# Optimization experiments

Hardware: AMD Instinct MI355X
Metric: run time of the kernel (lower is better)

## Reference

```python
import jax, jax.numpy as jnp
import numpy as np

N = 100000        # nodes
E = 1600000       # edges
G = 128           # graphs in batch
D_FEAT = 240      # continuous node features (input_features - 1)
EMB = 16          # node-type embedding dim
H = 256           # hidden size (both layers)
PH = 128          # pool / classifier hidden
GF = 32           # global feature dim
LN_EPS = 1e-5


def setup_inputs() -> dict:
    key = jax.random.key(0)
    ks = jax.random.split(key, 24)

    node_types = jax.random.randint(ks[0], (N,), 0, 400).astype(jnp.float32)
    feats = jax.random.normal(ks[1], (N, D_FEAT), dtype=jnp.float32)
    x = jnp.concatenate([node_types[:, None], feats], axis=1)  # [N, 241]

    edge_index = jax.random.randint(ks[2], (2, E), 0, N, dtype=jnp.int32)
    batch = jnp.sort(jax.random.randint(ks[3], (N,), 0, G, dtype=jnp.int32))
    global_features = jax.random.normal(ks[4], (G, GF), dtype=jnp.float32)

    s = 0.05
    p = {}
    p['emb_table'] = jax.random.normal(ks[5], (400, EMB), dtype=jnp.float32) * s
    # layer 0 GIN MLP (in=256 -> 256 -> 256) + LayerNorm
    p['l0_w1'] = jax.random.normal(ks[6], (H, H), dtype=jnp.float32) * s
    p['l0_b1'] = jnp.zeros((H,), jnp.float32)
    p['l0_w2'] = jax.random.normal(ks[7], (H, H), dtype=jnp.float32) * s
    p['l0_b2'] = jnp.zeros((H,), jnp.float32)
    p['ln0_g'] = jnp.ones((H,), jnp.float32)
    p['ln0_b'] = jnp.zeros((H,), jnp.float32)
    # layer 1
    p['l1_w1'] = jax.random.normal(ks[8], (H, H), dtype=jnp.float32) * s
    p['l1_b1'] = jnp.zeros((H,), jnp.float32)
    p['l1_w2'] = jax.random.normal(ks[9], (H, H), dtype=jnp.float32) * s
    p['l1_b2'] = jnp.zeros((H,), jnp.float32)
    p['ln1_g'] = jnp.ones((H,), jnp.float32)
    p['ln1_b'] = jnp.zeros((H,), jnp.float32)
    # attentional aggregation gate: 256 -> 128 -> 1
    p['gate_w1'] = jax.random.normal(ks[10], (H, PH), dtype=jnp.float32) * s
    p['gate_b1'] = jnp.zeros((PH,), jnp.float32)
    p['gate_w2'] = jax.random.normal(ks[11], (PH, 1), dtype=jnp.float32) * s
    p['gate_b2'] = jnp.zeros((1,), jnp.float32)
    # classifier: 256+32 -> 128 -> 2
    p['cls_w1'] = jax.random.normal(ks[12], (H + GF, PH), dtype=jnp.float32) * s
    p['cls_b1'] = jnp.zeros((PH,), jnp.float32)
    p['cls_w2'] = jax.random.normal(ks[13], (PH, 2), dtype=jnp.float32) * s
    p['cls_b2'] = jnp.zeros((2,), jnp.float32)

    return dict(x=x, edge_index=edge_index, batch=batch,
                global_features=global_features, **p)


def _layernorm(z, g, b):
    mu = jnp.mean(z, axis=-1, keepdims=True)
    var = jnp.mean(jnp.square(z - mu), axis=-1, keepdims=True)
    return (z - mu) * jax.lax.rsqrt(var + LN_EPS) * g + b


def _gin_block(h, src, dst, w1, b1, w2, b2, ln_g, ln_b):
    # GINConv, eps=0: mlp((1+eps)*x_i + sum_{j->i} x_j)
    agg = jax.ops.segment_sum(h[src], dst, num_segments=h.shape[0])
    z = h + agg
    z = jax.nn.relu(z @ w1 + b1) @ w2 + b2
    z = jax.nn.relu(_layernorm(z, ln_g, ln_b))
    return h + z  # dropout is identity in eval; residual


def reference(x, edge_index, batch, global_features, emb_table,
              l0_w1, l0_b1, l0_w2, l0_b2, ln0_g, ln0_b,
              l1_w1, l1_b1, l1_w2, l1_b2, ln1_g, ln1_b,
              gate_w1, gate_b1, gate_w2, gate_b2,
              cls_w1, cls_b1, cls_w2, cls_b2):
    node_types = x[:, 0].astype(jnp.int32)
    h = jnp.concatenate([x[:, 1:], emb_table[node_types]], axis=1)  # [N, 256]

    src, dst = edge_index[0], edge_index[1]
    h = _gin_block(h, src, dst, l0_w1, l0_b1, l0_w2, l0_b2, ln0_g, ln0_b)
    h = _gin_block(h, src, dst, l1_w1, l1_b1, l1_w2, l1_b2, ln1_g, ln1_b)

    # AttentionalAggregation: segment softmax over gate scores, weighted sum
    gate = jax.nn.relu(h @ gate_w1 + gate_b1) @ gate_w2 + gate_b2  # [N, 1]
    gate = gate[:, 0]
    m = jax.ops.segment_max(gate, batch, num_segments=G)
    a = jnp.exp(gate - m[batch])
    s = jax.ops.segment_sum(a, batch, num_segments=G)
    w = a / s[batch]
    pooled = jax.ops.segment_sum(w[:, None] * h, batch, num_segments=G)  # [G, 256]

    z = jnp.concatenate([pooled, global_features], axis=1)  # [G, 288]
    out = jax.nn.relu(z @ cls_w1 + cls_b1) @ cls_w2 + cls_b2  # [G, 2]
    return out
```

## Files before the change

### kernel.cpp

```cpp
#include <hip/hip_runtime.h>
#include <math.h>

#define N_NODES 100000
#define N_EDGES 1600000
#define NG      128
#define HD      256
#define PHD     128
#define GFD     32
#define XW      241
#define LN_EPS  1e-5f
#define SLOT    64

typedef __attribute__((ext_vector_type(8))) short bf8_t;
typedef __attribute__((ext_vector_type(4))) float f4_t;

static __device__ __forceinline__ float relu_f(float x){ return fmaxf(x, 0.0f); }

static __device__ __forceinline__ unsigned short f2bf_rn(float v) {
    unsigned int u = __float_as_uint(v);
    unsigned int r = (u + 0x7fffu + ((u >> 16) & 1u)) >> 16;
    return (unsigned short)r;
}
static __device__ __forceinline__ float bf2f(unsigned short h) {
    return __uint_as_float((unsigned int)h << 16);
}

__global__ void build_h_kernel(const float* __restrict__ x, const float* __restrict__ emb,
                               float* __restrict__ h, unsigned short* __restrict__ h16)
{
    int node = blockIdx.x;
    int tid  = threadIdx.x;
    const float* xr = x + (size_t)node * XW;
    float v;
    if (tid < 240) {
        v = xr[1 + tid];
    } else {
        int t = (int)xr[0];
        v = emb[t * 16 + (tid - 240)];
    }
    h[(size_t)node * HD + tid] = v;
    h16[(size_t)node * HD + tid] = f2bf_rn(v);
}

__global__ void fill_slots_kernel(const int* __restrict__ src, const int* __restrict__ dst,
                                  int* __restrict__ cnt, int* __restrict__ col, int e)
{
    int i = blockIdx.x * blockDim.x + threadIdx.x;
    if (i < e) {
        int d = dst[i];
        int p = atomicAdd(&cnt[d], 1);
        if (p < SLOT) col[(size_t)d * SLOT + p] = src[i];
    }
}

static __device__ __forceinline__ void pack_one(const float* __restrict__ w, short* __restrict__ hi,
                                                int N, int fbase)
{
    int lane = threadIdx.x & 63;
    int f = fbase * 4 + (threadIdx.x >> 6);
    const int KB = 8;
    int nb = f / KB, kb = f % KB;
    int n = nb * 16 + (lane & 15);
    int k0 = kb * 32 + (lane >> 4) * 8;
    size_t o = (size_t)f * 512 + lane * 8;
    #pragma unroll
    for (int j = 0; j < 8; j++) {
        float v = w[(size_t)(k0 + j) * N + n];
        hi[o + j] = (short)f2bf_rn(v);
    }
}

__global__ __launch_bounds__(256) void pack_all_kernel(
    const float* __restrict__ w0, const float* __restrict__ w1,
    const float* __restrict__ w2, const float* __restrict__ w3,
    const float* __restrict__ w4,
    short* o0h, short* o1h, short* o2h, short* o3h, short* o4h)
{
    int b = blockIdx.x;
    if      (b < 32)  pack_one(w0, o0h, HD,  b);
    else if (b < 64)  pack_one(w1, o1h, HD,  b - 32);
    else if (b < 96)  pack_one(w2, o2h, HD,  b - 64);
    else if (b < 128) pack_one(w3, o3h, HD,  b - 96);
    else              pack_one(w4, o4h, PHD, b - 128);
}

static __device__ __forceinline__ void mm32(
    f4_t (&acc)[2][4], const char* buf,
    const short* __restrict__ Bh,
    int wc, int cb, int kg, int lane)
{
    bf8_t bcur[4], bnxt[4];
    #pragma unroll
    for (int ni = 0; ni < 4; ni++)
        bcur[ni] = *(const bf8_t*)&Bh[((size_t)((wc*4+ni)*8))*512 + lane*8];
    for (int kb = 0; kb < 8; kb++) {
        if (kb < 7) {
            #pragma unroll
            for (int ni = 0; ni < 4; ni++)
                bnxt[ni] = *(const bf8_t*)&Bh[((size_t)((wc*4+ni)*8 + kb+1))*512 + lane*8];
        }
        bf8_t ahi[2], alo[2];
        #pragma unroll
        for (int mi = 0; mi < 2; mi++) {
            int row = mi*16 + cb;
            int byte = (row*512 + kb*64 + kg*16) ^ ((row & 7) << 4);
            ahi[mi] = *(const bf8_t*)(buf + byte);
            alo[mi] = *(const bf8_t*)(buf + 16384 + byte);
        }
        #pragma unroll
        for (int mi = 0; mi < 2; mi++)
            #pragma unroll
            for (int ni = 0; ni < 4; ni++)
                acc[mi][ni] = __builtin_amdgcn_mfma_f32_16x16x32_bf16(ahi[mi], bcur[ni], acc[mi][ni], 0, 0, 0);
        #pragma unroll
        for (int mi = 0; mi < 2; mi++)
            #pragma unroll
            for (int ni = 0; ni < 4; ni++)
                acc[mi][ni] = __builtin_amdgcn_mfma_f32_16x16x32_bf16(alo[mi], bcur[ni], acc[mi][ni], 0, 0, 0);
        #pragma unroll
        for (int ni = 0; ni < 4; ni++) bcur[ni] = bnxt[ni];
    }
}

__global__ __launch_bounds__(256, 4) void gin_layer_kernel(
    float* __restrict__ h, const unsigned short* __restrict__ h16i,
    unsigned short* __restrict__ h16o,
    const int* __restrict__ cnt, const int* __restrict__ col,
    const short* __restrict__ w1h, const float* __restrict__ b1,
    const short* __restrict__ w2h, const float* __restrict__ b2,
    const float* __restrict__ lng, const float* __restrict__ lnb)
{
    __shared__ char buf[32768];
    const int tid  = threadIdx.x;
    const int lane = tid & 63;
    const int wv   = tid >> 6;
    const int cb   = lane & 15;
    const int kg   = lane >> 4;
    const int l4   = lane * 4;
    const long row0 = (long)blockIdx.x * 32;

    for (int rr = 0; rr < 8; rr++) {
        int row = wv * 8 + rr;
        long grow = row0 + row;
        float4 a0 = *(const float4*)&h[grow * HD + l4];
        float4 a1 = make_float4(0,0,0,0), a2 = make_float4(0,0,0,0), a3 = make_float4(0,0,0,0);
        int deg = cnt[grow]; if (deg > SLOT) deg = SLOT;
        const int* cb4 = col + (size_t)grow * SLOT;
        int e = 0;
        for (; e + 4 <= deg; e += 4) {
            int s0 = cb4[e], s1 = cb4[e+1], s2 = cb4[e+2], s3 = cb4[e+3];
            ushort4 u0 = *(const ushort4*)&h16i[(size_t)s0 * HD + l4];
            ushort4 u1 = *(const ushort4*)&h16i[(size_t)s1 * HD + l4];
            ushort4 u2 = *(const ushort4*)&h16i[(size_t)s2 * HD + l4];
            ushort4 u3 = *(const ushort4*)&h16i[(size_t)s3 * HD + l4];
            a0.x += bf2f(u0.x); a0.y += bf2f(u0.y); a0.z += bf2f(u0.z); a0.w += bf2f(u0.w);
            a1.x += bf2f(u1.x); a1.y += bf2f(u1.y); a1.z += bf2f(u1.z); a1.w += bf2f(u1.w);
            a2.x += bf2f(u2.x); a2.y += bf2f(u2.y); a2.z += bf2f(u2.z); a2.w += bf2f(u2.w);
            a3.x += bf2f(u3.x); a3.y += bf2f(u3.y); a3.z += bf2f(u3.z); a3.w += bf2f(u3.w);
        }
        for (; e < deg; e++) {
            int s = cb4[e];
            ushort4 u = *(const ushort4*)&h16i[(size_t)s * HD + l4];
            a0.x += bf2f(u.x); a0.y += bf2f(u.y); a0.z += bf2f(u.z); a0.w += bf2f(u.w);
        }
        a0.x += a1.x + a2.x + a3.x;
        a0.y += a1.y + a2.y + a3.y;
        a0.z += a1.z + a2.z + a3.z;
        a0.w += a1.w + a2.w + a3.w;
        ushort4 hi4, lo4;
        unsigned short hb;
        hb = f2bf_rn(a0.x); hi4.x = hb; lo4.x = f2bf_rn(a0.x - bf2f(hb));
        hb = f2bf_rn(a0.y); hi4.y = hb; lo4.y = f2bf_rn(a0.y - bf2f(hb));
        hb = f2bf_rn(a0.z); hi4.z = hb; lo4.z = f2bf_rn(a0.z - bf2f(hb));
        hb = f2bf_rn(a0.w); hi4.w = hb; lo4.w = f2bf_rn(a0.w - bf2f(hb));
        int byte = (row * 512 + lane * 8) ^ ((row & 7) << 4);
        *(ushort4*)(buf + byte)         = hi4;
        *(ushort4*)(buf + 16384 + byte) = lo4;
    }
    __syncthreads();

    f4_t acc[2][4];
    const f4_t zero4 = {0.f, 0.f, 0.f, 0.f};
    #pragma unroll
    for (int mi = 0; mi < 2; mi++)
        #pragma unroll
        for (int ni = 0; ni < 4; ni++) acc[mi][ni] = zero4;

    mm32(acc, buf, w1h, wv, cb, kg, lane);
    __syncthreads();

    {
        float bias1[4];
        #pragma unroll
        for (int ni = 0; ni < 4; ni++) bias1[ni] = b1[wv * 64 + ni * 16 + cb];
        #pragma unroll
        for (int mi = 0; mi < 2; mi++) {
            #pragma unroll
            for (int ni = 0; ni < 4; ni++) {
                int colx2 = (wv * 64 + ni * 16 + cb) * 2;
                #pragma unroll
                for (int j = 0; j < 4; j++) {
                    float t = relu_f(acc[mi][ni][j] + bias1[ni]);
                    int row = mi * 16 + kg * 4 + j;
                    unsigned short hb = f2bf_rn(t);
                    unsigned short lb = f2bf_rn(t - bf2f(hb));
                    int byte = (row * 512 + colx2) ^ ((row & 7) << 4);
                    *(short*)(buf + byte)         = (short)hb;
                    *(short*)(buf + 16384 + byte) = (short)lb;
                }
            }
        }
    }
    __syncthreads();

    #pragma unroll
    for (int mi = 0; mi < 2; mi++)
        #pragma unroll
        for (int ni = 0; ni < 4; ni++) acc[mi][ni] = zero4;

    mm32(acc, buf, w2h, wv, cb, kg, lane);
    __syncthreads();

    {
        float bias2[4];
        #pragma unroll
        for (int ni = 0; ni < 4; ni++) bias2[ni] = b2[wv * 64 + ni * 16 + cb];
        #pragma unroll
        for (int mi = 0; mi < 2; mi++) {
            #pragma unroll
            for (int ni = 0; ni < 4; ni++) {
                int col2 = wv * 64 + ni * 16 + cb;
                #pragma unroll
                for (int j = 0; j < 4; j++) {
                    int row = mi * 16 + kg * 4 + j;
                    int byte = (row * 1024 + col2 * 4) ^ (((row >> 2) & 3) << 6);
                    *(float*)(buf + byte) = acc[mi][ni][j] + bias2[ni];
                }
            }
        }
    }
    __syncthreads();

    {
        const float4 gv = *(const float4*)&lng[l4];
        const float4 bv = *(const float4*)&lnb[l4];
        for (int rr = 0; rr < 8; rr++) {
            int row = wv * 8 + rr;
            long grow = row0 + row;
            int byte = (row * 1024 + lane * 16) ^ (((row >> 2) & 3) << 6);
            float4 v = *(const float4*)(buf + byte);
            float s = v.x + v.y + v.z + v.w;
            float q = v.x * v.x + v.y * v.y + v.z * v.z + v.w * v.w;
            #pragma unroll
            for (int off = 32; off > 0; off >>= 1) {
                s += __shfl_xor(s, off, 64);
                q += __shfl_xor(q, off, 64);
            }
            float mu = s * (1.0f / 256.0f);
            float var = q * (1.0f / 256.0f) - mu * mu;
            float rstd = rsqrtf(var + LN_EPS);
            size_t gi = (size_t)grow * HD + l4;
            float4 hv = *(float4*)&h[gi];
            hv.x += relu_f((v.x - mu) * rstd * gv.x + bv.x);
            hv.y += relu_f((v.y - mu) * rstd * gv.y + bv.y);
            hv.z += relu_f((v.z - mu) * rstd * gv.z + bv.z);
            hv.w += relu_f((v.w - mu) * rstd * gv.w + bv.w);
            *(float4*)&h[gi] = hv;
            ushort4 m16;
            m16.x = f2bf_rn(hv.x); m16.y = f2bf_rn(hv.y);
            m16.z = f2bf_rn(hv.z); m16.w = f2bf_rn(hv.w);
            *(ushort4*)&h16o[gi] = m16;
        }
    }
}

__global__ __launch_bounds__(256, 2) void gate_mfma_kernel(
    const float* __restrict__ h,
    const short* __restrict__ g1h, const float* __restrict__ gb1,
    const float* __restrict__ gw2, const float* __restrict__ gb2,
    float* __restrict__ gate)
{
    __shared__ char buf[65536];
    const int tid  = threadIdx.x;
    const int lane = tid & 63;
    const int wv   = tid >> 6;
    const int cb   = lane & 15;
    const int kg   = lane >> 4;
    const long row0 = (long)blockIdx.x * 64;

    for (int rr = 0; rr < 16; rr++) {
        int row = wv * 16 + rr;
        long grow = row0 + row;
        float4 v = make_float4(0.f, 0.f, 0.f, 0.f);
        if (grow < N_NODES) v = *(const float4*)&h[grow * HD + lane * 4];
        ushort4 hi4, lo4;
        unsigned short hb;
        hb = f2bf_rn(v.x); hi4.x = hb; lo4.x = f2bf_rn(v.x - bf2f(hb));
        hb = f2bf_rn(v.y); hi4.y = hb; lo4.y = f2bf_rn(v.y - bf2f(hb));
        hb = f2bf_rn(v.z); hi4.z = hb; lo4.z = f2bf_rn(v.z - bf2f(hb));
        hb = f2bf_rn(v.w); hi4.w = hb; lo4.w = f2bf_rn(v.w - bf2f(hb));
        int byte = (row * 512 + lane * 8) ^ ((row & 7) << 4);
        *(ushort4*)(buf + byte)         = hi4;
        *(ushort4*)(buf + 32768 + byte) = lo4;
    }
    __syncthreads();

    f4_t acc[4][2];
    const f4_t zero4 = {0.f, 0.f, 0.f, 0.f};
    #pragma unroll
    for (int mi = 0; mi < 4; mi++) { acc[mi][0] = zero4; acc[mi][1] = zero4; }

    #pragma unroll
    for (int pass = 0; pass < 2; pass++) {
        const char* Abase = (pass == 1) ? (buf + 32768) : buf;
        for (int kb = 0; kb < 8; kb++) {
            bf8_t a[4], b[2];
            #pragma unroll
            for (int mi = 0; mi < 4; mi++) {
                int row = mi * 16 + cb;
                int byte = (row * 512 + kb * 64 + kg * 16) ^ ((row & 7) << 4);
                a[mi] = *(const bf8_t*)(Abase + byte);
            }
            #pragma unroll
            for (int ni = 0; ni < 2; ni++) {
                int nb = wv * 2 + ni;
                b[ni] = *(const bf8_t*)&g1h[(size_t)(nb * 8 + kb) * 512 + lane * 8];
            }
            #pragma unroll
            for (int mi = 0; mi < 4; mi++)
                #pragma unroll
                for (int ni = 0; ni < 2; ni++)
                    acc[mi][ni] = __builtin_amdgcn_mfma_f32_16x16x32_bf16(a[mi], b[ni], acc[mi][ni], 0, 0, 0);
        }
    }
    __syncthreads();

    {
        float* G1 = (float*)buf;
        float bias1[2];
        bias1[0] = gb1[wv * 32 + cb];
        bias1[1] = gb1[wv * 32 + 16 + cb];
        #pragma unroll
        for (int mi = 0; mi < 4; mi++) {
            #pragma unroll
            for (int ni = 0; ni < 2; ni++) {
                int colv = wv * 32 + ni * 16 + cb;
                #pragma unroll
                for (int j = 0; j < 4; j++) {
                    int row = mi * 16 + kg * 4 + j;
                    G1[row * PHD + colv] = relu_f(acc[mi][ni][j] + bias1[ni]);
                }
            }
        }
    }
    __syncthreads();

    {
        const float* G1 = (const float*)buf;
        float2 wv2 = *(const float2*)&gw2[lane * 2];
        float b2v = gb2[0];
        for (int rr = 0; rr < 16; rr++) {
            int row = wv * 16 + rr;
            long grow = row0 + row;
            if (grow >= N_NODES) break;
            float2 t2 = *(const float2*)&G1[row * PHD + lane * 2];
            float p = t2.x * wv2.x + t2.y * wv2.y;
            #pragma unroll
            for (int off = 32; off > 0; off >>= 1) p += __shfl_xor(p, off, 64);
            if (lane == 0) gate[grow] = p + b2v;
        }
    }
}

__global__ void goff_kernel(const int* __restrict__ batch, int* __restrict__ goff, int n)
{
    int t = threadIdx.x;
    if (t > NG) return;
    int lo = 0, hi = n;
    while (lo < hi) {
        int mid = (lo + hi) >> 1;
        if (batch[mid] < t) lo = mid + 1; else hi = mid;
    }
    goff[t] = lo;
}

__global__ __launch_bounds__(256) void pool_kernel(
    const float* __restrict__ h, const float* __restrict__ gate,
    const int* __restrict__ goff, float* __restrict__ pooled)
{
    __shared__ float red[256];
    __shared__ float m_sh, s_sh;
    int g = blockIdx.x >> 2, q = blockIdx.x & 3;
    int tid = threadIdx.x;
    int beg = goff[g], end = goff[g + 1];
    if (beg >= end) return;

    float lm = -3.4e38f;
    for (int i = beg + tid; i < end; i += 256) lm = fmaxf(lm, gate[i]);
    red[tid] = lm; __syncthreads();
    for (int off = 128; off > 0; off >>= 1) {
        if (tid < off) red[tid] = fmaxf(red[tid], red[tid + off]);
        __syncthreads();
    }
    if (tid == 0) m_sh = red[0];
    __syncthreads();
    float m = m_sh;

    float ls = 0.0f;
    for (int i = beg + tid; i < end; i += 256) ls += expf(gate[i] - m);
    __syncthreads();
    red[tid] = ls; __syncthreads();
    for (int off = 128; off > 0; off >>= 1) {
        if (tid < off) red[tid] += red[tid + off];
        __syncthreads();
    }
    if (tid == 0) s_sh = red[0];
    __syncthreads();
    float inv_s = 1.0f / s_sh;

    float acc = 0.0f;
    for (int i = beg + q; i < end; i += 4) {
        float a = expf(gate[i] - m);
        acc += a * h[(size_t)i * HD + tid];
    }
    atomicAdd(&pooled[(size_t)g * HD + tid], acc * inv_s);
}

__global__ __launch_bounds__(128) void cls_kernel(
    const float* __restrict__ pooled, const float* __restrict__ gf,
    const float* __restrict__ w1, const float* __restrict__ b1,
    const float* __restrict__ w2, const float* __restrict__ b2,
    float* __restrict__ out)
{
    __shared__ float r0[128], r1[128];
    int g = blockIdx.x, c = threadIdx.x;
    float acc = b1[c];
    const float* pr = pooled + (size_t)g * HD;
    for (int k = 0; k < HD; k++) acc += pr[k] * w1[k * PHD + c];
    const float* gr = gf + g * GFD;
    for (int k = 0; k < GFD; k++) acc += gr[k] * w1[(HD + k) * PHD + c];
    float t = relu_f(acc);
    r0[c] = t * w2[c * 2 + 0];
    r1[c] = t * w2[c * 2 + 1];
    __syncthreads();
    for (int off = 64; off > 0; off >>= 1) {
        if (c < off) { r0[c] += r0[c + off]; r1[c] += r1[c + off]; }
        __syncthreads();
    }
    if (c == 0) {
        out[g * 2 + 0] = r0[0] + b2[0];
        out[g * 2 + 1] = r1[0] + b2[1];
    }
}

extern "C" void kernel_launch(void* const* d_in, const int* in_sizes, int n_in,
                              void* d_out, int out_size, void* d_ws, size_t ws_size,
                              hipStream_t stream)
{
    const float* x    = (const float*)d_in[0];
    const int*   ei   = (const int*)d_in[1];
    const int*   bat  = (const int*)d_in[2];
    const float* gf   = (const float*)d_in[3];
    const float* emb  = (const float*)d_in[4];
    const float* l0w1 = (const float*)d_in[5];
    const float* l0b1 = (const float*)d_in[6];
    const float* l0w2 = (const float*)d_in[7];
    const float* l0b2 = (const float*)d_in[8];
    const float* ln0g = (const float*)d_in[9];
    const float* ln0b = (const float*)d_in[10];
    const float* l1w1 = (const float*)d_in[11];
    const float* l1b1 = (const float*)d_in[12];
    const float* l1w2 = (const float*)d_in[13];
    const float* l1b2 = (const float*)d_in[14];
    const float* ln1g = (const float*)d_in[15];
    const float* ln1b = (const float*)d_in[16];
    const float* gw1  = (const float*)d_in[17];
    const float* gb1  = (const float*)d_in[18];
    const float* gw2  = (const float*)d_in[19];
    const float* gb2  = (const float*)d_in[20];
    const float* cw1  = (const float*)d_in[21];
    const float* cb1  = (const float*)d_in[22];
    const float* cw2  = (const float*)d_in[23];
    const float* cb2  = (const float*)d_in[24];

    char* ws = (char*)d_ws;
    size_t off = 0;
    auto alloc = [&](size_t bytes) {
        void* p = ws + off;
        off += (bytes + 255) & ~(size_t)255;
        return p;
    };
    float* h      = (float*)alloc((size_t)N_NODES * HD * 4);
    unsigned short* h16a = (unsigned short*)alloc((size_t)N_NODES * HD * 2);
    unsigned short* h16b = (unsigned short*)alloc((size_t)N_NODES * HD * 2);
    float* gate   = (float*)alloc((size_t)N_NODES * 4);
    int*   cnt    = (int*)alloc((size_t)N_NODES * 4);
    int*   col    = (int*)alloc((size_t)N_NODES * SLOT * 4);
    int*   goff   = (int*)alloc((NG + 1) * 4);
    float* pooled = (float*)alloc((size_t)NG * HD * 4);
    short* p_l0w1h = (short*)alloc((size_t)HD * HD * 2);
    short* p_l0w2h = (short*)alloc((size_t)HD * HD * 2);
    short* p_l1w1h = (short*)alloc((size_t)HD * HD * 2);
    short* p_l1w2h = (short*)alloc((size_t)HD * HD * 2);
    short* p_gw1h  = (short*)alloc((size_t)HD * PHD * 2);

    const int* src = ei;
    const int* dst = ei + N_EDGES;

    build_h_kernel<<<N_NODES, 256, 0, stream>>>(x, emb, h, h16a);

    hipMemsetAsync(cnt, 0, (size_t)N_NODES * 4, stream);
    fill_slots_kernel<<<(N_EDGES + 255) / 256, 256, 0, stream>>>(src, dst, cnt, col, N_EDGES);

    pack_all_kernel<<<144, 256, 0, stream>>>(l0w1, l0w2, l1w1, l1w2, gw1,
                                             p_l0w1h, p_l0w2h, p_l1w1h, p_l1w2h, p_gw1h);

    const int layer_grid = N_NODES / 32;

    gin_layer_kernel<<<layer_grid, 256, 0, stream>>>(h, h16a, h16b, cnt, col,
                                                     p_l0w1h, l0b1, p_l0w2h, l0b2, ln0g, ln0b);
    gin_layer_kernel<<<layer_grid, 256, 0, stream>>>(h, h16b, h16a, cnt, col,
                                                     p_l1w1h, l1b1, p_l1w2h, l1b2, ln1g, ln1b);

    gate_mfma_kernel<<<(N_NODES + 63) / 64, 256, 0, stream>>>(h, p_gw1h, gb1, gw2, gb2, gate);
    goff_kernel<<<1, 256, 0, stream>>>(bat, goff, N_NODES);
    hipMemsetAsync(pooled, 0, (size_t)NG * HD * 4, stream);
    pool_kernel<<<NG * 4, 256, 0, stream>>>(h, gate, goff, pooled);
    cls_kernel<<<NG, 128, 0, stream>>>(pooled, gf, cw1, cb1, cw2, cb2, (float*)d_out);
}
```

Before: 769.7 us.

## Use single-bf16 pass for second GIN matmul and raise occupancy bound

The intermediate activation after the first MLP layer is now stored as a single bf16 value instead of a hi/lo bf16 split, and the second matmul uses a new one-pass MFMA routine, halving MFMA work and LDS traffic for that GEMM. Launch bounds move from 4 to 5 blocks per CU to allow more occupancy, and the CSR slot fill uses nontemporal stores. The trade is reduced accuracy in the second matmul and possible register pressure from the tighter launch bound.

```diff
diff --git a/kernel.cpp b/kernel.cpp
--- a/kernel.cpp
+++ b/kernel.cpp
@@ -49,7 +49,7 @@
     if (i < e) {
         int d = dst[i];
         int p = atomicAdd(&cnt[d], 1);
-        if (p < SLOT) col[(size_t)d * SLOT + p] = src[i];
+        if (p < SLOT) __builtin_nontemporal_store(src[i], &col[(size_t)d * SLOT + p]);
     }
 }
 
@@ -122,7 +122,39 @@
     }
 }
 
-__global__ __launch_bounds__(256, 4) void gin_layer_kernel(
+static __device__ __forceinline__ void mm32_1p(
+    f4_t (&acc)[2][4], const char* buf,
+    const short* __restrict__ Bh,
+    int wc, int cb, int kg, int lane)
+{
+    bf8_t bcur[4], bnxt[4];
+    #pragma unroll
+    for (int ni = 0; ni < 4; ni++)
+        bcur[ni] = *(const bf8_t*)&Bh[((size_t)((wc*4+ni)*8))*512 + lane*8];
+    for (int kb = 0; kb < 8; kb++) {
+        if (kb < 7) {
+            #pragma unroll
+            for (int ni = 0; ni < 4; ni++)
+                bnxt[ni] = *(const bf8_t*)&Bh[((size_t)((wc*4+ni)*8 + kb+1))*512 + lane*8];
+        }
+        bf8_t ahi[2];
+        #pragma unroll
+        for (int mi = 0; mi < 2; mi++) {
+            int row = mi*16 + cb;
+            int byte = (row*512 + kb*64 + kg*16) ^ ((row & 7) << 4);
+            ahi[mi] = *(const bf8_t*)(buf + byte);
+        }
+        #pragma unroll
+        for (int mi = 0; mi < 2; mi++)
+            #pragma unroll
+            for (int ni = 0; ni < 4; ni++)
+                acc[mi][ni] = __builtin_amdgcn_mfma_f32_16x16x32_bf16(ahi[mi], bcur[ni], acc[mi][ni], 0, 0, 0);
+        #pragma unroll
+        for (int ni = 0; ni < 4; ni++) bcur[ni] = bnxt[ni];
+    }
+}
+
+__global__ __launch_bounds__(256, 5) void gin_layer_kernel(
     float* __restrict__ h, const unsigned short* __restrict__ h16i,
     unsigned short* __restrict__ h16o,
     const int* __restrict__ cnt, const int* __restrict__ col,
@@ -202,11 +234,8 @@
                 for (int j = 0; j < 4; j++) {
                     float t = relu_f(acc[mi][ni][j] + bias1[ni]);
                     int row = mi * 16 + kg * 4 + j;
-                    unsigned short hb = f2bf_rn(t);
-                    unsigned short lb = f2bf_rn(t - bf2f(hb));
                     int byte = (row * 512 + colx2) ^ ((row & 7) << 4);
-                    *(short*)(buf + byte)         = (short)hb;
-                    *(short*)(buf + 16384 + byte) = (short)lb;
+                    *(short*)(buf + byte) = (short)f2bf_rn(t);
                 }
             }
         }
@@ -218,7 +247,7 @@
         #pragma unroll
         for (int ni = 0; ni < 4; ni++) acc[mi][ni] = zero4;
 
-    mm32(acc, buf, w2h, wv, cb, kg, lane);
+    mm32_1p(acc, buf, w2h, wv, cb, kg, lane);
     __syncthreads();
 
     {
```

Result: slower. 852.6 us (+10.8%).
